# Kernel tuning notes

Measured on AMD Instinct MI355X. Metric: run time of the kernel, lower is better.

Reference implementation:

```python
import math
import jax, jax.numpy as jnp
import numpy as np

TWO_PI = 2.0 * math.pi


def cyclic_catmull_rom(phase, num_cp):
    """Returns (indices [B,4] int32, weights [B,4] float)."""
    pos = jnp.remainder(phase, TWO_PI) * (num_cp / TWO_PI)
    base = jnp.floor(pos).astype(jnp.int32)
    t = pos - base.astype(pos.dtype)
    t2 = t * t
    t3 = t2 * t
    idx = jnp.stack([
        jnp.remainder(base - 1, num_cp),
        jnp.remainder(base, num_cp),
        jnp.remainder(base + 1, num_cp),
        jnp.remainder(base + 2, num_cp),
    ], axis=1)
    w = jnp.stack([
        -0.5 * t + t2 - 0.5 * t3,
        1.0 - 2.5 * t2 + 1.5 * t3,
        0.5 * t + 2.0 * t2 - 1.5 * t3,
        -0.5 * t2 + 0.5 * t3,
    ], axis=1)
    return idx, w


def setup_inputs() -> dict:
    key = jax.random.key(0)
    ks = jax.random.split(key, 10)
    B = 16384
    INPUT_DIM = 33          # phase + 32 state features
    STATE = 32
    EXP = 128               # expanded_input_dim
    PN = 8                  # phase_node_count
    C = 8                   # phase_control_points
    H1, H2 = 256, 256
    OUT = 16
    FIRST_IN = EXP + PN + STATE          # 168
    PF_IN = H1 + STATE                   # 288

    def xavier(k, shape):
        fan_out, fan_in = shape[-2], shape[-1]
        lim = math.sqrt(6.0 / (fan_in + fan_out))
        return jax.random.uniform(k, shape, jnp.float32, -lim, lim)

    return {
        "inputs": jax.random.normal(ks[0], (B, INPUT_DIM), jnp.float32),
        "exp_w": xavier(ks[1], (EXP, STATE)),
        "exp_b": jnp.zeros((EXP,), jnp.float32),
        "phase_node_cp": 0.02 * jax.random.normal(ks[2], (C, PN), jnp.float32),
        "w1": xavier(ks[3], (H1, FIRST_IN)),
        "b1": jnp.zeros((H1,), jnp.float32),
        "pf_w": xavier(ks[4], (C, H2, PF_IN)),
        "pf_b": jnp.zeros((C, H2), jnp.float32),
        "w_out": xavier(ks[5], (OUT, H2 + STATE)),
        "b_out": jnp.zeros((OUT,), jnp.float32),
    }


def reference(inputs, exp_w, exp_b, phase_node_cp, w1, b1, pf_w, pf_b, w_out, b_out):
    num_cp = pf_w.shape[0]
    phase = inputs[:, 0]
    state = inputs[:, 1:]                                  # [B, S]

    expanded = jax.nn.elu(state @ exp_w.T + exp_b)          # [B, EXP]

    idx, w = cyclic_catmull_rom(phase, num_cp)              # [B,4], [B,4]
    phase_nodes = jnp.sum(w[:, :, None] * phase_node_cp[idx], axis=1)  # [B, PN]

    h1 = jax.nn.elu(jnp.concatenate([expanded, phase_nodes, state], axis=1) @ w1.T + b1)
    h2_in = jnp.concatenate([h1, state], axis=1)            # [B, PF_IN]

    # Phase-functioned linear: compute matvec against every control matrix,
    # then gather + blend the 4 relevant ones (same math as blending weight
    # matrices first, by linearity; avoids the [B,4,OUT,IN] intermediate).
    z = jnp.einsum('bi,coi->bco', h2_in, pf_w)              # [B, C, H2]
    z4 = jnp.take_along_axis(z, idx[:, :, None], axis=1)    # [B, 4, H2]
    b4 = pf_b[idx]                                          # [B, 4, H2]
    h2 = jax.nn.elu(jnp.sum(w[:, :, None] * (z4 + b4), axis=1))

    return jnp.concatenate([h2, state], axis=1) @ w_out.T + b_out
```

## Files before the change

### kernel.cpp

```cpp
#include <hip/hip_runtime.h>
#include <math.h>

typedef short bf16x8 __attribute__((ext_vector_type(8)));
typedef float f32x4 __attribute__((ext_vector_type(4)));

#define MFMA16(a, b, c) __builtin_amdgcn_mfma_f32_16x16x32_bf16((a), (b), (c), 0, 0, 0)

#define TWO_PI_F 6.28318530717958647692f

#define PFW_OFF   0
#define PFW_ELEMS (8 * 256 * 296)
#define W1_OFF    (PFW_OFF + PFW_ELEMS)
#define W1_ELEMS  (256 * 200)
#define EXPW_OFF  (W1_OFF + W1_ELEMS)
#define EXPW_ELEMS (128 * 40)
#define WOUT_OFF  (EXPW_OFF + EXPW_ELEMS)
#define WOUT_ELEMS (16 * 296)
#define TOTAL_ELEMS (WOUT_OFF + WOUT_ELEMS)

#define MAIN_THREADS 512
#define TILE_B 64

__device__ __forceinline__ unsigned short f2bf(float x) {
    unsigned int u = __float_as_uint(x);
    unsigned int r = u + 0x7fffu + ((u >> 16) & 1u);
    return (unsigned short)(r >> 16);
}

__device__ __forceinline__ float elu_f(float x) {
    return x > 0.0f ? x : (expf(x) - 1.0f);
}

__global__ __launch_bounds__(256) void prep_weights(
    const float* __restrict__ exp_w, const float* __restrict__ w1,
    const float* __restrict__ pf_w, const float* __restrict__ w_out,
    unsigned short* __restrict__ wsb)
{
    int i = blockIdx.x * blockDim.x + threadIdx.x;
    if (i >= TOTAL_ELEMS) return;
    float v;
    if (i < W1_OFF) {
        int k = i % 296;
        int co = i / 296;
        v = (k < 288) ? pf_w[(size_t)co * 288 + k] : 0.0f;
    } else if (i < EXPW_OFF) {
        int j = i - W1_OFF;
        int k = j % 200, o = j / 200;
        v = (k < 168) ? w1[o * 168 + k] : 0.0f;
    } else if (i < WOUT_OFF) {
        int j = i - EXPW_OFF;
        int k = j % 40, o = j / 40;
        v = (k < 32) ? exp_w[o * 32 + k] : 0.0f;
    } else {
        int j = i - WOUT_OFF;
        int k = j % 296, o = j / 296;
        v = (k < 288) ? w_out[o * 288 + k] : 0.0f;
    }
    wsb[i] = f2bf(v);
}

__global__ __launch_bounds__(MAIN_THREADS, 2) void pfnn_mfma(
    const float* __restrict__ inputs,
    const float* __restrict__ exp_b,
    const float* __restrict__ cp,
    const float* __restrict__ b1,
    const float* __restrict__ pf_b,
    const float* __restrict__ b_out,
    const unsigned short* __restrict__ wsb,
    float* __restrict__ out, int B)
{
    __shared__ unsigned short buf1[TILE_B * 296];
    __shared__ unsigned short buf2[TILE_B * 296];
    __shared__ float sWcT[8][TILE_B];

    const unsigned short* pfwb  = wsb + PFW_OFF;
    const unsigned short* w1b   = wsb + W1_OFF;
    const unsigned short* expwb = wsb + EXPW_OFF;
    const unsigned short* woutb = wsb + WOUT_OFF;

    const int t    = threadIdx.x;
    const int w    = t >> 6;
    const int lane = t & 63;
    const int cfr  = lane & 15;
    const int kg   = lane >> 4;
    const int b0   = blockIdx.x * TILE_B;

    for (int i = t; i < TILE_B * 32; i += MAIN_THREADS) {
        int row = i >> 5, j = i & 31;
        int grow = b0 + row;
        float v = (grow < B) ? inputs[(size_t)grow * 33 + 1 + j] : 0.0f;
        unsigned short bv = f2bf(v);
        buf1[row * 296 + 136 + j] = bv;
        buf1[row * 296 + 256 + j] = bv;
        buf2[row * 296 + 256 + j] = bv;
        buf1[row * 296 + 168 + j] = 0;
    }
    if (t < TILE_B) {
        int grow = b0 + t;
        float ph = (grow < B) ? inputs[(size_t)grow * 33] : 0.0f;
        float p = fmodf(ph, TWO_PI_F);
        if (p < 0.0f) p += TWO_PI_F;
        float pos = p * (8.0f / TWO_PI_F);
        int base = (int)floorf(pos);
        float tt = pos - (float)base;
        base &= 7;
        float t2 = tt * tt, t3 = t2 * tt;
        float cw0 = -0.5f * tt + t2 - 0.5f * t3;
        float cw1 = 1.0f - 2.5f * t2 + 1.5f * t3;
        float cw2 = 0.5f * tt + 2.0f * t2 - 1.5f * t3;
        float cw3 = -0.5f * t2 + 0.5f * t3;
        int i0 = (base + 7) & 7, i1 = base, i2 = (base + 1) & 7, i3 = (base + 2) & 7;
        #pragma unroll
        for (int c = 0; c < 8; ++c) sWcT[c][t] = 0.0f;
        sWcT[i0][t] += cw0;
        sWcT[i1][t] += cw1;
        sWcT[i2][t] += cw2;
        sWcT[i3][t] += cw3;
        #pragma unroll
        for (int j = 0; j < 8; ++j) {
            float pn = cw0 * cp[i0 * 8 + j] + cw1 * cp[i1 * 8 + j]
                     + cw2 * cp[i2 * 8 + j] + cw3 * cp[i3 * 8 + j];
            buf1[t * 296 + 128 + j] = f2bf(pn);
        }
    }
    __syncthreads();

    {
        const int n0 = w * 16;
        bf16x8 bw = *(const bf16x8*)(expwb + (n0 + cfr) * 40 + kg * 8);
        const f32x4 zero = {0.f, 0.f, 0.f, 0.f};
        f32x4 acc[4];
        #pragma unroll
        for (int m = 0; m < 4; ++m) {
            bf16x8 a = *(const bf16x8*)&buf1[(m * 16 + cfr) * 296 + 136 + kg * 8];
            acc[m] = MFMA16(a, bw, zero);
        }
        float bias = exp_b[n0 + cfr];
        #pragma unroll
        for (int m = 0; m < 4; ++m)
            #pragma unroll
            for (int r = 0; r < 4; ++r) {
                int row = m * 16 + kg * 4 + r;
                buf1[row * 296 + n0 + cfr] = f2bf(elu_f(acc[m][r] + bias));
            }
    }
    __syncthreads();

    {
        const int n0 = w * 32;
        f32x4 acc[2][4];
        #pragma unroll
        for (int nt = 0; nt < 2; ++nt)
            #pragma unroll
            for (int m = 0; m < 4; ++m)
                acc[nt][m] = (f32x4){0.f, 0.f, 0.f, 0.f};
        #pragma unroll
        for (int kk = 0; kk < 6; ++kk) {
            bf16x8 a[4];
            #pragma unroll
            for (int m = 0; m < 4; ++m)
                a[m] = *(const bf16x8*)&buf1[(m * 16 + cfr) * 296 + kk * 32 + kg * 8];
            #pragma unroll
            for (int nt = 0; nt < 2; ++nt) {
                bf16x8 bw = *(const bf16x8*)(w1b + (n0 + nt * 16 + cfr) * 200 + kk * 32 + kg * 8);
                #pragma unroll
                for (int m = 0; m < 4; ++m)
                    acc[nt][m] = MFMA16(a[m], bw, acc[nt][m]);
            }
        }
        #pragma unroll
        for (int nt = 0; nt < 2; ++nt) {
            float bias = b1[n0 + nt * 16 + cfr];
            #pragma unroll
            for (int m = 0; m < 4; ++m)
                #pragma unroll
                for (int r = 0; r < 4; ++r) {
                    int row = m * 16 + kg * 4 + r;
                    buf2[row * 296 + n0 + nt * 16 + cfr] = f2bf(elu_f(acc[nt][m][r] + bias));
                }
        }
    }
    __syncthreads();

    {
        const int o0 = w * 32;
        f32x4 h2acc[2][4];
        #pragma unroll
        for (int nt = 0; nt < 2; ++nt)
            #pragma unroll
            for (int m = 0; m < 4; ++m)
                h2acc[nt][m] = (f32x4){0.f, 0.f, 0.f, 0.f};

        for (int c = 0; c < 8; ++c) {
            const unsigned short* wp0 =
                pfwb + (size_t)(c * 256 + o0 + cfr) * 296 + kg * 8;
            const unsigned short* wp1 = wp0 + 16 * 296;

            f32x4 z[2][4];
            #pragma unroll
            for (int nt = 0; nt < 2; ++nt)
                #pragma unroll
                for (int m = 0; m < 4; ++m)
                    z[nt][m] = (f32x4){0.f, 0.f, 0.f, 0.f};

            #pragma unroll
            for (int kk = 0; kk < 9; ++kk) {
                bf16x8 b0 = *(const bf16x8*)(wp0 + kk * 32);
                bf16x8 b1 = *(const bf16x8*)(wp1 + kk * 32);
                #pragma unroll
                for (int m = 0; m < 4; ++m) {
                    bf16x8 a = *(const bf16x8*)&buf2[(m * 16 + cfr) * 296 + kk * 32 + kg * 8];
                    z[0][m] = MFMA16(a, b0, z[0][m]);
                    z[1][m] = MFMA16(a, b1, z[1][m]);
                }
            }

            float pfb0 = pf_b[c * 256 + o0 + cfr];
            float pfb1 = pf_b[c * 256 + o0 + 16 + cfr];
            #pragma unroll
            for (int m = 0; m < 4; ++m) {
                f32x4 wcv = *(const f32x4*)&sWcT[c][m * 16 + kg * 4];
                #pragma unroll
                for (int r = 0; r < 4; ++r) {
                    h2acc[0][m][r] += wcv[r] * (z[0][m][r] + pfb0);
                    h2acc[1][m][r] += wcv[r] * (z[1][m][r] + pfb1);
                }
            }
        }
        #pragma unroll
        for (int nt = 0; nt < 2; ++nt)
            #pragma unroll
            for (int m = 0; m < 4; ++m)
                #pragma unroll
                for (int r = 0; r < 4; ++r) {
                    int row = m * 16 + kg * 4 + r;
                    buf1[row * 296 + o0 + nt * 16 + cfr] = f2bf(elu_f(h2acc[nt][m][r]));
                }
    }
    __syncthreads();

    if (w < 4) {
        f32x4 acc = {0.f, 0.f, 0.f, 0.f};
        #pragma unroll
        for (int kk = 0; kk < 9; ++kk) {
            bf16x8 a  = *(const bf16x8*)&buf1[(w * 16 + cfr) * 296 + kk * 32 + kg * 8];
            bf16x8 bw = *(const bf16x8*)(woutb + cfr * 296 + kk * 32 + kg * 8);
            acc = MFMA16(a, bw, acc);
        }
        float bias = b_out[cfr];
        #pragma unroll
        for (int r = 0; r < 4; ++r) {
            int grow = b0 + w * 16 + kg * 4 + r;
            if (grow < B) out[(size_t)grow * 16 + cfr] = acc[r] + bias;
        }
    }
}

#define FB_TILE 16
#define FB_THREADS 256

__global__ __launch_bounds__(FB_THREADS) void pfnn_fused_f32(
    const float* __restrict__ inputs,
    const float* __restrict__ exp_w, const float* __restrict__ exp_b,
    const float* __restrict__ cp,
    const float* __restrict__ w1, const float* __restrict__ b1,
    const float* __restrict__ pf_w, const float* __restrict__ pf_b,
    const float* __restrict__ w_out, const float* __restrict__ b_out,
    float* __restrict__ out, int B)
{
    __shared__ float sState[FB_TILE][36];
    __shared__ float sFI[FB_TILE][172];
    __shared__ float sH2in[FB_TILE][292];
    __shared__ float sH2[FB_TILE][260];
    __shared__ float sWc[FB_TILE][8];
    __shared__ float sPhase[FB_TILE];

    const int t = threadIdx.x;
    const int b0 = blockIdx.x * FB_TILE;
    const int nb = min(FB_TILE, B - b0);

    for (int i = t; i < nb * 33; i += FB_THREADS) {
        int b = i / 33, j = i % 33;
        float v = inputs[(size_t)(b0 + b) * 33 + j];
        if (j == 0) sPhase[b] = v;
        else { sState[b][j-1] = v; sFI[b][136 + j-1] = v; sH2in[b][256 + j-1] = v; }
    }
    for (int i = nb * 33 + t; i < FB_TILE * 33; i += FB_THREADS) {
        int b = i / 33, j = i % 33;
        if (j == 0) sPhase[b] = 0.0f;
        else { sState[b][j-1] = 0.0f; sFI[b][136 + j-1] = 0.0f; sH2in[b][256 + j-1] = 0.0f; }
    }
    __syncthreads();
    {
        const int o = t & 127;
        const int bh = t >> 7;
        const float4* wrow = reinterpret_cast<const float4*>(exp_w + o * 32);
        float4 wv[8];
        #pragma unroll
        for (int q = 0; q < 8; ++q) wv[q] = wrow[q];
        const float bias = exp_b[o];
        for (int bi = bh; bi < FB_TILE; bi += 2) {
            float acc = bias;
            #pragma unroll
            for (int q = 0; q < 8; ++q) {
                acc += wv[q].x * sState[bi][q*4+0] + wv[q].y * sState[bi][q*4+1]
                     + wv[q].z * sState[bi][q*4+2] + wv[q].w * sState[bi][q*4+3];
            }
            sFI[bi][o] = elu_f(acc);
        }
    }
    if (t < FB_TILE) {
        float p = fmodf(sPhase[t], TWO_PI_F);
        if (p < 0.0f) p += TWO_PI_F;
        float pos = p * (8.0f / TWO_PI_F);
        int base = (int)floorf(pos);
        float tt = pos - (float)base;
        base &= 7;
        float t2 = tt*tt, t3 = t2*tt;
        float cw0 = -0.5f*tt + t2 - 0.5f*t3;
        float cw1 = 1.0f - 2.5f*t2 + 1.5f*t3;
        float cw2 = 0.5f*tt + 2.0f*t2 - 1.5f*t3;
        float cw3 = -0.5f*t2 + 0.5f*t3;
        int i0 = (base+7)&7, i1 = base, i2 = (base+1)&7, i3 = (base+2)&7;
        #pragma unroll
        for (int c = 0; c < 8; ++c) sWc[t][c] = 0.0f;
        sWc[t][i0] += cw0; sWc[t][i1] += cw1; sWc[t][i2] += cw2; sWc[t][i3] += cw3;
        #pragma unroll
        for (int j = 0; j < 8; ++j)
            sFI[t][128 + j] = cw0*cp[i0*8+j] + cw1*cp[i1*8+j] + cw2*cp[i2*8+j] + cw3*cp[i3*8+j];
    }
    __syncthreads();
    {
        const int o = t;
        float acc[FB_TILE];
        const float bias = b1[o];
        #pragma unroll
        for (int b = 0; b < FB_TILE; ++b) acc[b] = bias;
        const float* wrow = w1 + o * 168;
        for (int k4 = 0; k4 < 42; ++k4) {
            float4 wv = *reinterpret_cast<const float4*>(wrow + k4 * 4);
            #pragma unroll
            for (int b = 0; b < FB_TILE; ++b) {
                float4 a = *reinterpret_cast<const float4*>(&sFI[b][k4 * 4]);
                acc[b] += wv.x*a.x + wv.y*a.y + wv.z*a.z + wv.w*a.w;
            }
        }
        #pragma unroll
        for (int b = 0; b < FB_TILE; ++b) sH2in[b][o] = elu_f(acc[b]);
    }
    __syncthreads();
    {
        const int o = t;
        float h2acc[FB_TILE];
        #pragma unroll
        for (int b = 0; b < FB_TILE; ++b) h2acc[b] = 0.0f;
        for (int g = 0; g < 2; ++g) {
            float zacc[FB_TILE][4];
            #pragma unroll
            for (int b = 0; b < FB_TILE; ++b)
                #pragma unroll
                for (int ci = 0; ci < 4; ++ci) zacc[b][ci] = 0.0f;
            for (int k4 = 0; k4 < 72; ++k4) {
                float wv[4][4];
                #pragma unroll
                for (int ci = 0; ci < 4; ++ci) {
                    float4 v = *reinterpret_cast<const float4*>(
                        pf_w + (size_t)((g*4+ci) * 256 + o) * 288 + k4 * 4);
                    wv[ci][0]=v.x; wv[ci][1]=v.y; wv[ci][2]=v.z; wv[ci][3]=v.w;
                }
                #pragma unroll
                for (int b = 0; b < FB_TILE; ++b) {
                    float4 a = *reinterpret_cast<const float4*>(&sH2in[b][k4 * 4]);
                    #pragma unroll
                    for (int ci = 0; ci < 4; ++ci)
                        zacc[b][ci] += a.x*wv[ci][0] + a.y*wv[ci][1] + a.z*wv[ci][2] + a.w*wv[ci][3];
                }
            }
            #pragma unroll
            for (int b = 0; b < FB_TILE; ++b)
                #pragma unroll
                for (int ci = 0; ci < 4; ++ci)
                    h2acc[b] += sWc[b][g*4+ci] * (zacc[b][ci] + pf_b[(g*4+ci) * 256 + o]);
        }
        #pragma unroll
        for (int b = 0; b < FB_TILE; ++b) sH2[b][o] = elu_f(h2acc[b]);
    }
    __syncthreads();
    {
        const int b = t >> 4;
        const int j = t & 15;
        const float* wrow = w_out + j * 288;
        float acc = b_out[j];
        for (int k4 = 0; k4 < 64; ++k4) {
            float4 wv = *reinterpret_cast<const float4*>(wrow + k4 * 4);
            float4 a = *reinterpret_cast<const float4*>(&sH2[b][k4 * 4]);
            acc += wv.x*a.x + wv.y*a.y + wv.z*a.z + wv.w*a.w;
        }
        #pragma unroll
        for (int j2 = 0; j2 < 32; ++j2) acc += wrow[256 + j2] * sState[b][j2];
        if (b < nb) out[(size_t)(b0 + b) * 16 + j] = acc;
    }
}

extern "C" void kernel_launch(void* const* d_in, const int* in_sizes, int n_in,
                              void* d_out, int out_size, void* d_ws, size_t ws_size,
                              hipStream_t stream) {
    const float* inputs = (const float*)d_in[0];
    const float* exp_w  = (const float*)d_in[1];
    const float* exp_b  = (const float*)d_in[2];
    const float* cp     = (const float*)d_in[3];
    const float* w1     = (const float*)d_in[4];
    const float* b1     = (const float*)d_in[5];
    const float* pf_w   = (const float*)d_in[6];
    const float* pf_b   = (const float*)d_in[7];
    const float* w_out  = (const float*)d_in[8];
    const float* b_out  = (const float*)d_in[9];
    float* out = (float*)d_out;

    const int B = in_sizes[0] / 33;

    if (d_ws != nullptr && ws_size >= (size_t)TOTAL_ELEMS * sizeof(unsigned short)) {
        unsigned short* wsb = (unsigned short*)d_ws;
        prep_weights<<<(TOTAL_ELEMS + 255) / 256, 256, 0, stream>>>(
            exp_w, w1, pf_w, w_out, wsb);
        pfnn_mfma<<<(B + TILE_B - 1) / TILE_B, MAIN_THREADS, 0, stream>>>(
            inputs, exp_b, cp, b1, pf_b, b_out, wsb, out, B);
    } else {
        pfnn_fused_f32<<<(B + FB_TILE - 1) / FB_TILE, FB_THREADS, 0, stream>>>(
            inputs, exp_w, exp_b, cp, w1, b1, pf_w, pf_b, w_out, b_out, out, B);
    }
}
```

Baseline: 47.00 us.

## Double block to 16 waves, giving each wave one 16-column output tile

The block grows from 512 to 1024 threads, so each of the 16 waves owns a single 16-wide column tile in the hidden and phase-function layers instead of two. In the expansion layer the waves are split across row halves. The aim is more waves in flight to hide latency, with fewer accumulators per wave. In exchange, each A fragment read from LDS now feeds only one MFMA instead of two, which doubles LDS traffic per MFMA. The launch bound of 4 blocks of 1024 threads is probably unreachable given LDS use per block.

After: 150.7 us. +220.7%, slower.

```diff
diff --git a/kernel.cpp b/kernel.cpp
--- a/kernel.cpp
+++ b/kernel.cpp
@@ -18,7 +18,7 @@
 #define WOUT_ELEMS (16 * 296)
 #define TOTAL_ELEMS (WOUT_OFF + WOUT_ELEMS)
 
-#define MAIN_THREADS 512
+#define MAIN_THREADS 1024
 #define TILE_B 64
 
 __device__ __forceinline__ unsigned short f2bf(float x) {
@@ -59,7 +59,7 @@
     wsb[i] = f2bf(v);
 }
 
-__global__ __launch_bounds__(MAIN_THREADS, 2) void pfnn_mfma(
+__global__ __launch_bounds__(MAIN_THREADS, 4) void pfnn_mfma(
     const float* __restrict__ inputs,
     const float* __restrict__ exp_b,
     const float* __restrict__ cp,
@@ -126,116 +126,95 @@
     __syncthreads();
 
     {
-        const int n0 = w * 16;
+        const int n0 = (w & 7) * 16;
+        const int mh = w >> 3;
         bf16x8 bw = *(const bf16x8*)(expwb + (n0 + cfr) * 40 + kg * 8);
         const f32x4 zero = {0.f, 0.f, 0.f, 0.f};
-        f32x4 acc[4];
-        #pragma unroll
-        for (int m = 0; m < 4; ++m) {
+        f32x4 acc[2];
+        #pragma unroll
+        for (int mi = 0; mi < 2; ++mi) {
+            int m = mh * 2 + mi;
             bf16x8 a = *(const bf16x8*)&buf1[(m * 16 + cfr) * 296 + 136 + kg * 8];
-            acc[m] = MFMA16(a, bw, zero);
+            acc[mi] = MFMA16(a, bw, zero);
         }
         float bias = exp_b[n0 + cfr];
         #pragma unroll
-        for (int m = 0; m < 4; ++m)
+        for (int mi = 0; mi < 2; ++mi) {
+            int m = mh * 2 + mi;
             #pragma unroll
             for (int r = 0; r < 4; ++r) {
                 int row = m * 16 + kg * 4 + r;
-                buf1[row * 296 + n0 + cfr] = f2bf(elu_f(acc[m][r] + bias));
-            }
-    }
-    __syncthreads();
-
-    {
-        const int n0 = w * 32;
-        f32x4 acc[2][4];
-        #pragma unroll
-        for (int nt = 0; nt < 2; ++nt)
-            #pragma unroll
-            for (int m = 0; m < 4; ++m)
-                acc[nt][m] = (f32x4){0.f, 0.f, 0.f, 0.f};
+                buf1[row * 296 + n0 + cfr] = f2bf(elu_f(acc[mi][r] + bias));
+            }
+        }
+    }
+    __syncthreads();
+
+    {
+        const int n0 = w * 16;
+        f32x4 acc[4];
+        #pragma unroll
+        for (int m = 0; m < 4; ++m) acc[m] = (f32x4){0.f, 0.f, 0.f, 0.f};
         #pragma unroll
         for (int kk = 0; kk < 6; ++kk) {
-            bf16x8 a[4];
-            #pragma unroll
-            for (int m = 0; m < 4; ++m)
-                a[m] = *(const bf16x8*)&buf1[(m * 16 + cfr) * 296 + kk * 32 + kg * 8];
-            #pragma unroll
-            for (int nt = 0; nt < 2; ++nt) {
-                bf16x8 bw = *(const bf16x8*)(w1b + (n0 + nt * 16 + cfr) * 200 + kk * 32 + kg * 8);
-                #pragma unroll
-                for (int m = 0; m < 4; ++m)
-                    acc[nt][m] = MFMA16(a[m], bw, acc[nt][m]);
-            }
-        }
-        #pragma unroll
-        for (int nt = 0; nt < 2; ++nt) {
-            float bias = b1[n0 + nt * 16 + cfr];
-            #pragma unroll
-            for (int m = 0; m < 4; ++m)
-                #pragma unroll
-                for (int r = 0; r < 4; ++r) {
-                    int row = m * 16 + kg * 4 + r;
-                    buf2[row * 296 + n0 + nt * 16 + cfr] = f2bf(elu_f(acc[nt][m][r] + bias));
-                }
-        }
-    }
-    __syncthreads();
-
-    {
-        const int o0 = w * 32;
-        f32x4 h2acc[2][4];
-        #pragma unroll
-        for (int nt = 0; nt < 2; ++nt)
-            #pragma unroll
-            for (int m = 0; m < 4; ++m)
-                h2acc[nt][m] = (f32x4){0.f, 0.f, 0.f, 0.f};
+            bf16x8 bw = *(const bf16x8*)(w1b + (n0 + cfr) * 200 + kk * 32 + kg * 8);
+            #pragma unroll
+            for (int m = 0; m < 4; ++m) {
+                bf16x8 a = *(const bf16x8*)&buf1[(m * 16 + cfr) * 296 + kk * 32 + kg * 8];
+                acc[m] = MFMA16(a, bw, acc[m]);
+            }
+        }
+        float bias = b1[n0 + cfr];
+        #pragma unroll
+        for (int m = 0; m < 4; ++m)
+            #pragma unroll
+            for (int r = 0; r < 4; ++r) {
+                int row = m * 16 + kg * 4 + r;
+                buf2[row * 296 + n0 + cfr] = f2bf(elu_f(acc[m][r] + bias));
+            }
+    }
+    __syncthreads();
+
+    {
+        const int n0 = w * 16;
+        f32x4 h2acc[4];
+        #pragma unroll
+        for (int m = 0; m < 4; ++m) h2acc[m] = (f32x4){0.f, 0.f, 0.f, 0.f};
 
         for (int c = 0; c < 8; ++c) {
-            const unsigned short* wp0 =
-                pfwb + (size_t)(c * 256 + o0 + cfr) * 296 + kg * 8;
-            const unsigned short* wp1 = wp0 + 16 * 296;
-
-            f32x4 z[2][4];
-            #pragma unroll
-            for (int nt = 0; nt < 2; ++nt)
-                #pragma unroll
-                for (int m = 0; m < 4; ++m)
-                    z[nt][m] = (f32x4){0.f, 0.f, 0.f, 0.f};
+            const unsigned short* wp =
+                pfwb + (size_t)(c * 256 + n0 + cfr) * 296 + kg * 8;
+
+            f32x4 z[4];
+            #pragma unroll
+            for (int m = 0; m < 4; ++m) z[m] = (f32x4){0.f, 0.f, 0.f, 0.f};
 
             #pragma unroll
             for (int kk = 0; kk < 9; ++kk) {
-                bf16x8 b0 = *(const bf16x8*)(wp0 + kk * 32);
-                bf16x8 b1 = *(const bf16x8*)(wp1 + kk * 32);
+                bf16x8 bw = *(const bf16x8*)(wp + kk * 32);
                 #pragma unroll
                 for (int m = 0; m < 4; ++m) {
                     bf16x8 a = *(const bf16x8*)&buf2[(m * 16 + cfr) * 296 + kk * 32 + kg * 8];
-                    z[0][m] = MFMA16(a, b0, z[0][m]);
-                    z[1][m] = MFMA16(a, b1, z[1][m]);
+                    z[m] = MFMA16(a, bw, z[m]);
                 }
             }
 
-            float pfb0 = pf_b[c * 256 + o0 + cfr];
-            float pfb1 = pf_b[c * 256 + o0 + 16 + cfr];
+            float pfb = pf_b[c * 256 + n0 + cfr];
             #pragma unroll
             for (int m = 0; m < 4; ++m) {
                 f32x4 wcv = *(const f32x4*)&sWcT[c][m * 16 + kg * 4];
                 #pragma unroll
-                for (int r = 0; r < 4; ++r) {
-                    h2acc[0][m][r] += wcv[r] * (z[0][m][r] + pfb0);
-                    h2acc[1][m][r] += wcv[r] * (z[1][m][r] + pfb1);
-                }
-            }
-        }
-        #pragma unroll
-        for (int nt = 0; nt < 2; ++nt)
-            #pragma unroll
-            for (int m = 0; m < 4; ++m)
-                #pragma unroll
-                for (int r = 0; r < 4; ++r) {
-                    int row = m * 16 + kg * 4 + r;
-                    buf1[row * 296 + o0 + nt * 16 + cfr] = f2bf(elu_f(h2acc[nt][m][r]));
-                }
+                for (int r = 0; r < 4; ++r)
+                    h2acc[m][r] += wcv[r] * (z[m][r] + pfb);
+            }
+        }
+        #pragma unroll
+        for (int m = 0; m < 4; ++m)
+            #pragma unroll
+            for (int r = 0; r < 4; ++r) {
+                int row = m * 16 + kg * 4 + r;
+                buf1[row * 296 + n0 + cfr] = f2bf(elu_f(h2acc[m][r]));
+            }
     }
     __syncthreads();
 
```

## Stage phase-function weights into LDS with double-buffered async global loads

Applied to the files above, without the earlier changes.

The phase-functioned layer now copies each 64-row weight chunk (per control point and output slice) into a double-buffered LDS area with global_load_lds. The copy of the next chunk overlaps the MFMAs on the current one. The per-wave work is remapped to a 16-column by 32-row tile, so each weight fragment is read once from LDS and shared across waves, rather than every wave loading B fragments directly from global memory. This adds about 75KB of LDS, which may cut occupancy below the two blocks per CU implied by the launch bounds. It also adds a __syncthreads per chunk, 32 barriers in total.

Measured after the change: 62.83 us. 1.34x slower.

```diff
diff --git a/kernel.cpp b/kernel.cpp
--- a/kernel.cpp
+++ b/kernel.cpp
@@ -20,6 +20,7 @@
 
 #define MAIN_THREADS 512
 #define TILE_B 64
+#define CHUNK_BYTES (64 * 296 * 2)
 
 __device__ __forceinline__ unsigned short f2bf(float x) {
     unsigned int u = __float_as_uint(x);
@@ -29,6 +30,22 @@
 
 __device__ __forceinline__ float elu_f(float x) {
     return x > 0.0f ? x : (expf(x) - 1.0f);
+}
+
+__device__ __forceinline__ void gload_lds16(const void* g, void* l) {
+    __builtin_amdgcn_global_load_lds(
+        (const __attribute__((address_space(1))) void*)g,
+        (__attribute__((address_space(3))) void*)l, 16, 0, 0);
+}
+
+__device__ __forceinline__ void stage_chunk(const unsigned short* gsrc, unsigned short* ldst, int t) {
+    const char* g = (const char*)gsrc;
+    char* l = (char*)ldst;
+    #pragma unroll
+    for (int r = 0; r < 4; ++r)
+        gload_lds16(g + r * 8192 + t * 16, l + r * 8192 + t * 16);
+    if (t < 320)
+        gload_lds16(g + 4 * 8192 + t * 16, l + 4 * 8192 + t * 16);
 }
 
 __global__ __launch_bounds__(256) void prep_weights(
@@ -69,8 +86,9 @@
     const unsigned short* __restrict__ wsb,
     float* __restrict__ out, int B)
 {
-    __shared__ unsigned short buf1[TILE_B * 296];
-    __shared__ unsigned short buf2[TILE_B * 296];
+    __shared__ __align__(16) unsigned short buf1[TILE_B * 296];
+    __shared__ __align__(16) unsigned short buf2[TILE_B * 296];
+    __shared__ __align__(16) unsigned short wbuf[2][64 * 296];
     __shared__ float sWcT[8][TILE_B];
 
     const unsigned short* pfwb  = wsb + PFW_OFF;
@@ -84,6 +102,8 @@
     const int cfr  = lane & 15;
     const int kg   = lane >> 4;
     const int b0   = blockIdx.x * TILE_B;
+
+    stage_chunk(pfwb, wbuf[0], t);
 
     for (int i = t; i < TILE_B * 32; i += MAIN_THREADS) {
         int row = i >> 5, j = i & 31;
@@ -183,59 +203,52 @@
     __syncthreads();
 
     {
-        const int o0 = w * 32;
-        f32x4 h2acc[2][4];
-        #pragma unroll
-        for (int nt = 0; nt < 2; ++nt)
-            #pragma unroll
-            for (int m = 0; m < 4; ++m)
-                h2acc[nt][m] = (f32x4){0.f, 0.f, 0.f, 0.f};
-
-        for (int c = 0; c < 8; ++c) {
-            const unsigned short* wp0 =
-                pfwb + (size_t)(c * 256 + o0 + cfr) * 296 + kg * 8;
-            const unsigned short* wp1 = wp0 + 16 * 296;
-
-            f32x4 z[2][4];
-            #pragma unroll
-            for (int nt = 0; nt < 2; ++nt)
-                #pragma unroll
-                for (int m = 0; m < 4; ++m)
-                    z[nt][m] = (f32x4){0.f, 0.f, 0.f, 0.f};
-
-            #pragma unroll
-            for (int kk = 0; kk < 9; ++kk) {
-                bf16x8 b0 = *(const bf16x8*)(wp0 + kk * 32);
-                bf16x8 b1 = *(const bf16x8*)(wp1 + kk * 32);
-                #pragma unroll
-                for (int m = 0; m < 4; ++m) {
-                    bf16x8 a = *(const bf16x8*)&buf2[(m * 16 + cfr) * 296 + kk * 32 + kg * 8];
-                    z[0][m] = MFMA16(a, b0, z[0][m]);
-                    z[1][m] = MFMA16(a, b1, z[1][m]);
-                }
-            }
-
-            float pfb0 = pf_b[c * 256 + o0 + cfr];
-            float pfb1 = pf_b[c * 256 + o0 + 16 + cfr];
-            #pragma unroll
-            for (int m = 0; m < 4; ++m) {
-                f32x4 wcv = *(const f32x4*)&sWcT[c][m * 16 + kg * 4];
+        const int n_t = w & 3;
+        const int mh  = w >> 2;
+        int cur = 0;
+        for (int nch = 0; nch < 4; ++nch) {
+            f32x4 h2acc[2];
+            h2acc[0] = (f32x4){0.f, 0.f, 0.f, 0.f};
+            h2acc[1] = (f32x4){0.f, 0.f, 0.f, 0.f};
+            for (int c = 0; c < 8; ++c) {
+                const int idx = nch * 8 + c;
+                if (idx < 31) {
+                    const int nidx = idx + 1;
+                    const int nc = nidx & 7, nnch = nidx >> 3;
+                    stage_chunk(pfwb + (size_t)(nc * 256 + nnch * 64) * 296,
+                                wbuf[cur ^ 1], t);
+                }
+                f32x4 z[2];
+                z[0] = (f32x4){0.f, 0.f, 0.f, 0.f};
+                z[1] = (f32x4){0.f, 0.f, 0.f, 0.f};
+                #pragma unroll
+                for (int kk = 0; kk < 9; ++kk) {
+                    bf16x8 bw = *(const bf16x8*)&wbuf[cur][(n_t * 16 + cfr) * 296 + kk * 32 + kg * 8];
+                    #pragma unroll
+                    for (int mi = 0; mi < 2; ++mi) {
+                        bf16x8 a = *(const bf16x8*)&buf2[((mh * 2 + mi) * 16 + cfr) * 296 + kk * 32 + kg * 8];
+                        z[mi] = MFMA16(a, bw, z[mi]);
+                    }
+                }
+                float pfb = pf_b[c * 256 + nch * 64 + n_t * 16 + cfr];
+                #pragma unroll
+                for (int mi = 0; mi < 2; ++mi) {
+                    f32x4 wcv = *(const f32x4*)&sWcT[c][(mh * 2 + mi) * 16 + kg * 4];
+                    #pragma unroll
+                    for (int r = 0; r < 4; ++r)
+                        h2acc[mi][r] += wcv[r] * (z[mi][r] + pfb);
+                }
+                __syncthreads();
+                cur ^= 1;
+            }
+            #pragma unroll
+            for (int mi = 0; mi < 2; ++mi)
                 #pragma unroll
                 for (int r = 0; r < 4; ++r) {
-                    h2acc[0][m][r] += wcv[r] * (z[0][m][r] + pfb0);
-                    h2acc[1][m][r] += wcv[r] * (z[1][m][r] + pfb1);
-                }
-            }
-        }
-        #pragma unroll
-        for (int nt = 0; nt < 2; ++nt)
-            #pragma unroll
-            for (int m = 0; m < 4; ++m)
-                #pragma unroll
-                for (int r = 0; r < 4; ++r) {
-                    int row = m * 16 + kg * 4 + r;
-                    buf1[row * 296 + o0 + nt * 16 + cfr] = f2bf(elu_f(h2acc[nt][m][r]));
-                }
+                    int row = (mh * 2 + mi) * 16 + kg * 4 + r;
+                    buf1[row * 296 + nch * 64 + n_t * 16 + cfr] = f2bf(elu_f(h2acc[mi][r]));
+                }
+        }
     }
     __syncthreads();
 
```
